# Optimization experiments

Measured on AMD Instinct MI355X. Metric: run time of the kernel, lower is better.

The kernel has to match this reference:

```python
import jax, jax.numpy as jnp
import numpy as np

B, T, C, H = 8, 1024, 1024, 16
D = C // H
EPS = 1e-5

def _ln(x, g, b):
    mu = jnp.mean(x, axis=-1, keepdims=True)
    var = jnp.var(x, axis=-1, keepdims=True)
    return (x - mu) * jax.lax.rsqrt(var + EPS) * g + b

def _build_mask(cond_mask, cond_len, token_len):
    # Vectorized form of the per-batch Python-loop mask in the torch module.
    counts = jnp.sum(cond_mask, axis=-1)            # [B] number of valid cond tokens
    rows = jnp.arange(T)
    cols = jnp.arange(T)
    # all rows may attend to the first counts[i] (cond) columns
    m_cond = cols[None, None, :] < counts[:, None, None]          # [B,1,T]
    m_cond = jnp.broadcast_to(m_cond, (B, T, T))
    # block-causal tiled pattern on rows/cols >= cond_len:
    # value = (col - cond_len) % token_len <= (row - cond_len) % token_len
    pattern = ((cols[None, :] - cond_len) % token_len) <= ((rows[:, None] - cond_len) % token_len)
    m_block = (rows[:, None] >= cond_len) & (cols[None, :] >= cond_len) & pattern  # [T,T]
    # cols >= cond_len: overwritten by block pattern (rows < cond_len stay 0 there)
    mask = jnp.where(cols[None, None, :] < cond_len, m_cond, m_block[None, :, :])
    return mask[:, None, :, :]                      # [B,1,T,T] bool

def _attn(x, Wq, bq, Wk, bk, Wv, bv, Wp, bp, cond_mask, cond_len, token_len):
    q = (x @ Wq + bq).reshape(B, T, H, D).transpose(0, 2, 1, 3)  # [B,H,T,D]
    k = (x @ Wk + bk).reshape(B, T, H, D).transpose(0, 2, 1, 3)
    v = (x @ Wv + bv).reshape(B, T, H, D).transpose(0, 2, 1, 3)
    att = jnp.einsum('bhqd,bhkd->bhqk', q, k) * (1.0 / np.sqrt(D))
    mask = _build_mask(cond_mask, cond_len, token_len)
    att = jnp.where(mask, att, -jnp.inf)
    att = jax.nn.softmax(att, axis=-1)
    y = jnp.einsum('bhqk,bhkd->bhqd', att, v)
    y = y.transpose(0, 2, 1, 3).reshape(B, T, C)
    return y @ Wp + bp

def setup_inputs() -> dict:
    key = jax.random.key(0)
    ks = jax.random.split(key, 16)
    cond_len, token_len = 256, 768
    s = 1.0 / np.sqrt(C)
    counts = jax.random.randint(ks[0], (B,), 1, cond_len + 1)
    cond_mask = (jnp.arange(T)[None, :] < counts[:, None]).astype(jnp.int32)
    return {
        'x': jax.random.normal(ks[1], (B, T, C), jnp.float32),
        'ln1_g': jnp.ones((C,), jnp.float32), 'ln1_b': jnp.zeros((C,), jnp.float32),
        'Wq': jax.random.normal(ks[2], (C, C), jnp.float32) * s, 'bq': jnp.zeros((C,), jnp.float32),
        'Wk': jax.random.normal(ks[3], (C, C), jnp.float32) * s, 'bk': jnp.zeros((C,), jnp.float32),
        'Wv': jax.random.normal(ks[4], (C, C), jnp.float32) * s, 'bv': jnp.zeros((C,), jnp.float32),
        'Wp': jax.random.normal(ks[5], (C, C), jnp.float32) * s, 'bp': jnp.zeros((C,), jnp.float32),
        'ln2_g': jnp.ones((C,), jnp.float32), 'ln2_b': jnp.zeros((C,), jnp.float32),
        'W1': jax.random.normal(ks[6], (C, 4 * C), jnp.float32) * s, 'b1': jnp.zeros((4 * C,), jnp.float32),
        'W2': jax.random.normal(ks[7], (4 * C, C), jnp.float32) * (0.5 * s), 'b2': jnp.zeros((C,), jnp.float32),
        'cond_mask': cond_mask,
        'cond_len': cond_len,
        'token_len': token_len,
    }

def reference(x, ln1_g, ln1_b, Wq, bq, Wk, bk, Wv, bv, Wp, bp, ln2_g, ln2_b, W1, b1, W2, b2, cond_mask, cond_len, token_len):
    x = x + _attn(_ln(x, ln1_g, ln1_b), Wq, bq, Wk, bk, Wv, bv, Wp, bp, cond_mask, cond_len, token_len)
    h = _ln(x, ln2_g, ln2_b)
    x = x + (jax.nn.gelu(h @ W1 + b1, approximate=False) @ W2 + b2)
    return x
```

## Files before the change

kernel.cpp:

```cpp
#include <hip/hip_runtime.h>
#include <hip/hip_bf16.h>
#include <cstdint>
#include <cstddef>

typedef __attribute__((ext_vector_type(8))) short short8;
typedef __attribute__((ext_vector_type(4))) float f32x4;
typedef __attribute__((ext_vector_type(4))) unsigned short us4;

#define MFMA_BF16(a, b, c) __builtin_amdgcn_mfma_f32_16x16x32_bf16((a), (b), (c), 0, 0, 0)
#define VMCNT(n) asm volatile("s_waitcnt vmcnt(" #n ")" ::: "memory")

__device__ __forceinline__ unsigned short f2bf(float f) {
  unsigned int u = __float_as_uint(f);
  u += 0x7FFFu + ((u >> 16) & 1u);
  return (unsigned short)(u >> 16);
}

__device__ __forceinline__ float gelu_fast(float v) {
  const float u = v * (0.79788456f + 0.03567741f * v * v);
  const float e = exp2f(u * 2.88539008f);
  return v - v * __builtin_amdgcn_rcpf(e + 1.0f);
}

typedef const void __attribute__((address_space(1)))* as1_cvp;
typedef void __attribute__((address_space(3)))* as3_vp;
__device__ __forceinline__ void gll16(const short* g, short* l) {
#if defined(__HIP_DEVICE_COMPILE__)
  __builtin_amdgcn_global_load_lds((as1_cvp)g, (as3_vp)l, 16, 0, 0);
#else
  (void)g; (void)l;
#endif
}

__global__ void count_kernel(const int* __restrict__ cm, int* __restrict__ counts) {
  __shared__ int sd[256];
  const int b = blockIdx.x, t = threadIdx.x;
  int s = 0;
  for (int i = t; i < 1024; i += 256) s += cm[b * 1024 + i];
  sd[t] = s; __syncthreads();
  for (int k = 128; k > 0; k >>= 1) { if (t < k) sd[t] += sd[t + k]; __syncthreads(); }
  if (t == 0) counts[b] = sd[0];
}

__global__ void pack_bias_kernel(const float* __restrict__ bq, const float* __restrict__ bk,
                                 const float* __restrict__ bv, float* __restrict__ dst) {
  int i = blockIdx.x * 256 + threadIdx.x;
  dst[i] = (i < 1024) ? bq[i] : (i < 2048 ? bk[i - 1024] : bv[i - 2048]);
}

__global__ void transpose_kernel(const float* __restrict__ src, unsigned short* __restrict__ dst,
                                 int R, int C) {
  __shared__ float tile[32][33];
  const int c0 = blockIdx.x * 32, r0 = blockIdx.y * 32;
  const int tx = threadIdx.x, ty = threadIdx.y;
  #pragma unroll
  for (int i = ty; i < 32; i += 8)
    tile[i][tx] = src[(size_t)(r0 + i) * C + (c0 + tx)];
  __syncthreads();
  #pragma unroll
  for (int i = ty; i < 32; i += 8)
    dst[(size_t)(c0 + i) * R + (r0 + tx)] = f2bf(tile[tx][i]);
}

__global__ void vtrans_kernel(const short* __restrict__ qkv, short* __restrict__ vtr) {
  __shared__ short tile[32][33];
  const int bh = blockIdx.z;
  const int t0 = blockIdx.x * 32, d0 = blockIdx.y * 32;
  const int b = bh >> 4, h = bh & 15;
  const int tx = threadIdx.x, ty = threadIdx.y;
  const short* src = qkv + (size_t)b * 1024 * 3072 + 2048 + h * 64;
  #pragma unroll
  for (int i = ty; i < 32; i += 8)
    tile[i][tx] = src[(size_t)(t0 + i) * 3072 + d0 + tx];
  __syncthreads();
  short* dst = vtr + (size_t)bh * 65536;
  #pragma unroll
  for (int i = ty; i < 32; i += 8)
    dst[(d0 + i) * 1024 + t0 + tx] = tile[tx][i];
}

__global__ __launch_bounds__(256) void ln_kernel(const float* __restrict__ in,
                                                 const float* __restrict__ gw,
                                                 const float* __restrict__ bw,
                                                 unsigned short* __restrict__ out) {
  const int row = blockIdx.x, t = threadIdx.x;
  const float4 v = ((const float4*)(in + (size_t)row * 1024))[t];
  float s = v.x + v.y + v.z + v.w;
  float ss = v.x * v.x + v.y * v.y + v.z * v.z + v.w * v.w;
  #pragma unroll
  for (int o = 32; o >= 1; o >>= 1) { s += __shfl_down(s, o, 64); ss += __shfl_down(ss, o, 64); }
  __shared__ float red[8];
  if ((t & 63) == 0) { red[t >> 6] = s; red[4 + (t >> 6)] = ss; }
  __syncthreads();
  const float S  = red[0] + red[1] + red[2] + red[3];
  const float SS = red[4] + red[5] + red[6] + red[7];
  const float mu = S * (1.0f / 1024.0f);
  const float var = SS * (1.0f / 1024.0f) - mu * mu;
  const float rs = rsqrtf(var + 1e-5f);
  const int c = t * 4;
  const float4 g4 = ((const float4*)gw)[t];
  const float4 b4 = ((const float4*)bw)[t];
  us4 o4;
  o4[0] = f2bf((v.x - mu) * rs * g4.x + b4.x);
  o4[1] = f2bf((v.y - mu) * rs * g4.y + b4.y);
  o4[2] = f2bf((v.z - mu) * rs * g4.z + b4.z);
  o4[3] = f2bf((v.w - mu) * rs * g4.w + b4.w);
  *(us4*)(out + (size_t)row * 1024 + c) = o4;
}

template <int EPI>
__global__ __launch_bounds__(512, 1) void gemm_n256_kernel(
    const short* __restrict__ A, const short* __restrict__ BT,
    const float* __restrict__ bias, int N, int K, int gm,
    unsigned short* __restrict__ outb) {
  __shared__ alignas(16) short lds[73728];
  const int t = threadIdx.x;
  const int l = t & 63, w = t >> 6;
  const int lq = l & 15, g = l >> 4;
  const int wr = w >> 2, wc = w & 3;
  const int cpx = (int)gridDim.x >> 3;
  const int wid = ((int)blockIdx.x & 7) * cpx + ((int)blockIdx.x >> 3);
  const int bm = (wid % gm) * 128, bn = (wid / gm) * 256;
  const int NT = K >> 6;

  const int csw = ((t & 7) ^ ((t >> 3) & 7)) * 8;
  const int sr = t >> 3;

  const f32x4 z4 = {0.f, 0.f, 0.f, 0.f};
  f32x4 acc[4][4];
  #pragma unroll
  for (int i = 0; i < 4; i++)
    #pragma unroll
    for (int j = 0; j < 4; j++) acc[i][j] = z4;

  auto stageA = [&](int buf, int k0) {
    const short* src = A + (size_t)(bm + sr) * K + k0 + csw;
    short* dst = lds + buf * 24576 + t * 8;
    gll16(src, dst);
    gll16(src + (size_t)64 * K, dst + 4096);
  };
  auto stageB = [&](int buf, int h, int k0) {
    const short* src = BT + (size_t)(bn + h * 128 + sr) * K + k0 + csw;
    short* dst = lds + buf * 24576 + 8192 + h * 8192 + t * 8;
    gll16(src, dst);
    gll16(src + (size_t)64 * K, dst + 4096);
  };
  auto rdA = [&](int buf, int mi2, int kk) {
    const int ra = wr * 64 + mi2 * 16 + lq;
    const int unit = (kk * 4 + g) ^ (ra & 7);
    return *(const short8*)(lds + buf * 24576 + ra * 64 + unit * 8);
  };
  auto rdB = [&](int buf, int h, int ni2, int kk) {
    const int cb = wc * 32 + ni2 * 16 + lq;
    const int unit = (kk * 4 + g) ^ (cb & 7);
    return *(const short8*)(lds + buf * 24576 + 8192 + h * 8192 + cb * 64 + unit * 8);
  };

  stageA(0, 0);     stageB(0, 0, 0);
  stageB(0, 1, 0);
  stageA(1, 64);    stageB(1, 0, 64);
  VMCNT(4);
  __builtin_amdgcn_s_barrier();

  int cur = 0;
  for (int v = 0; v < NT; ++v) {
    const int nx1 = (cur == 2) ? 0 : cur + 1;
    const int nx2 = (nx1 == 2) ? 0 : nx1 + 1;
    short8 a[4][2], b[2][2], b2[2][2];
    #pragma unroll
    for (int mi2 = 0; mi2 < 4; ++mi2)
      #pragma unroll
      for (int kk = 0; kk < 2; ++kk) a[mi2][kk] = rdA(cur, mi2, kk);
    #pragma unroll
    for (int ni2 = 0; ni2 < 2; ++ni2)
      #pragma unroll
      for (int kk = 0; kk < 2; ++kk) b[ni2][kk] = rdB(cur, 0, ni2, kk);
    if (v + 1 < NT) stageB(nx1, 1, (v + 1) * 64);
    __builtin_amdgcn_s_setprio(1);
    #pragma unroll
    for (int mi2 = 0; mi2 < 4; ++mi2)
      #pragma unroll
      for (int ni2 = 0; ni2 < 2; ++ni2)
        #pragma unroll
        for (int kk = 0; kk < 2; ++kk)
          acc[mi2][ni2] = MFMA_BF16(a[mi2][kk], b[ni2][kk], acc[mi2][ni2]);
    __builtin_amdgcn_s_setprio(0);
    #pragma unroll
    for (int ni2 = 0; ni2 < 2; ++ni2)
      #pragma unroll
      for (int kk = 0; kk < 2; ++kk) b2[ni2][kk] = rdB(cur, 1, ni2, kk);
    if (v + 2 < NT) {
      stageA(nx2, (v + 2) * 64); stageB(nx2, 0, (v + 2) * 64);
      VMCNT(4);
    } else {
      VMCNT(0);
    }
    __builtin_amdgcn_s_barrier();
    __builtin_amdgcn_s_setprio(1);
    #pragma unroll
    for (int mi2 = 0; mi2 < 4; ++mi2)
      #pragma unroll
      for (int ni2 = 0; ni2 < 2; ++ni2)
        #pragma unroll
        for (int kk = 0; kk < 2; ++kk)
          acc[mi2][2 + ni2] = MFMA_BF16(a[mi2][kk], b2[ni2][kk], acc[mi2][2 + ni2]);
    __builtin_amdgcn_s_setprio(0);
    cur = nx1;
  }

  __syncthreads();
  unsigned short* eb = (unsigned short*)lds;
  #pragma unroll
  for (int mi2 = 0; mi2 < 4; ++mi2) {
    #pragma unroll
    for (int n = 0; n < 4; ++n) {
      const int col = (n >> 1) * 128 + wc * 32 + (n & 1) * 16 + lq;
      const float bv = bias[bn + col];
      #pragma unroll
      for (int r = 0; r < 4; ++r) {
        const int row = wr * 64 + mi2 * 16 + 4 * g + r;
        float vv = acc[mi2][n][r] + bv;
        if (EPI == 1) vv = gelu_fast(vv);
        eb[row * 256 + col] = f2bf(vv);
      }
    }
  }
  __syncthreads();
  #pragma unroll
  for (int it = 0; it < 8; ++it) {
    const int unit = it * 512 + t;
    const int row = unit >> 5, c8 = unit & 31;
    const short8 vv = *(const short8*)(lds + unit * 8);
    *(short8*)((short*)outb + (size_t)(bm + row) * N + bn + c8 * 8) = vv;
  }
}

template <int EPI>
__global__ __launch_bounds__(512, 1) void gemm_k2_kernel(
    const short* __restrict__ A, const short* __restrict__ BT,
    const float* __restrict__ bias, int N, int K, int gm,
    float* __restrict__ outf, const float* __restrict__ res) {
  __shared__ alignas(16) short lds[73728];
  const int t = threadIdx.x;
  const int l = t & 63, w = t >> 6;
  const int lq = l & 15, g = l >> 4;
  const int wr = w >> 2, wc = w & 3;
  const int cpx = (int)gridDim.x >> 3;
  const int wid = ((int)blockIdx.x & 7) * cpx + ((int)blockIdx.x >> 3);
  const int bm = (wid % gm) * 256, bn = (wid / gm) * 128;
  const int NT = K >> 6;

  const int csw = ((t & 7) ^ ((t >> 3) & 7)) * 8;
  const int sA = t >> 3;
  const int sB = ((t >> 8) & 1) * 64 + ((t >> 3) & 31);

  const f32x4 z4 = {0.f, 0.f, 0.f, 0.f};
  f32x4 acc[8][2];
  #pragma unroll
  for (int i = 0; i < 8; i++) { acc[i][0] = z4; acc[i][1] = z4; }

  auto stageA = [&](int buf, int h, int k0) {
    const short* src = A + (size_t)(bm + h * 64 + sA) * K + k0 + csw;
    short* dst = lds + buf * 24576 + h * 8192 + t * 8;
    gll16(src, dst);
    gll16(src + (size_t)128 * K, dst + 4096);
  };
  auto stageB = [&](int buf, int h, int k0) {
    const short* src = BT + (size_t)(bn + h * 32 + sB) * K + k0 + csw;
    short* dst = lds + buf * 24576 + 16384 + h * 4096 + t * 8;
    gll16(src, dst);
  };
  auto rdA = [&](int buf, int mh, int mi2, int kk) {
    const int ra = wr * 64 + mi2 * 16 + lq;
    const int unit = (kk * 4 + g) ^ (ra & 7);
    return *(const short8*)(lds + buf * 24576 + mh * 8192 + ra * 64 + unit * 8);
  };
  auto rdB = [&](int buf, int ni2, int kk) {
    const int h = wc & 1;
    const int rb = (wc >> 1) * 32 + ni2 * 16 + lq;
    const int unit = (kk * 4 + g) ^ (rb & 7);
    return *(const short8*)(lds + buf * 24576 + 16384 + h * 4096 + rb * 64 + unit * 8);
  };

  stageA(0, 0, 0);  stageB(0, 0, 0);
  stageA(0, 1, 0);  stageB(0, 1, 0);
  stageA(1, 0, 64); stageB(1, 0, 64);
  VMCNT(3);
  __builtin_amdgcn_s_barrier();

  int cur = 0;
  for (int v = 0; v < NT; ++v) {
    const int nx1 = (cur == 2) ? 0 : cur + 1;
    const int nx2 = (nx1 == 2) ? 0 : nx1 + 1;
    short8 a[4][2], b[2][2], a2[4][2];
    #pragma unroll
    for (int mi2 = 0; mi2 < 4; ++mi2)
      #pragma unroll
      for (int kk = 0; kk < 2; ++kk) a[mi2][kk] = rdA(cur, 0, mi2, kk);
    #pragma unroll
    for (int ni2 = 0; ni2 < 2; ++ni2)
      #pragma unroll
      for (int kk = 0; kk < 2; ++kk) b[ni2][kk] = rdB(cur, ni2, kk);
    if (v + 1 < NT) { stageA(nx1, 1, (v + 1) * 64); stageB(nx1, 1, (v + 1) * 64); }
    __builtin_amdgcn_s_setprio(1);
    #pragma unroll
    for (int mi2 = 0; mi2 < 4; ++mi2)
      #pragma unroll
      for (int ni2 = 0; ni2 < 2; ++ni2)
        #pragma unroll
        for (int kk = 0; kk < 2; ++kk)
          acc[mi2][ni2] = MFMA_BF16(a[mi2][kk], b[ni2][kk], acc[mi2][ni2]);
    __builtin_amdgcn_s_setprio(0);
    #pragma unroll
    for (int mi2 = 0; mi2 < 4; ++mi2)
      #pragma unroll
      for (int kk = 0; kk < 2; ++kk) a2[mi2][kk] = rdA(cur, 1, mi2, kk);
    if (v + 2 < NT) {
      stageA(nx2, 0, (v + 2) * 64); stageB(nx2, 0, (v + 2) * 64);
      VMCNT(3);
    } else {
      VMCNT(0);
    }
    __builtin_amdgcn_s_barrier();
    __builtin_amdgcn_s_setprio(1);
    #pragma unroll
    for (int mi2 = 0; mi2 < 4; ++mi2)
      #pragma unroll
      for (int ni2 = 0; ni2 < 2; ++ni2)
        #pragma unroll
        for (int kk = 0; kk < 2; ++kk)
          acc[4 + mi2][ni2] = MFMA_BF16(a2[mi2][kk], b[ni2][kk], acc[4 + mi2][ni2]);
    __builtin_amdgcn_s_setprio(0);
    cur = nx1;
  }

  #pragma unroll
  for (int mi = 0; mi < 8; ++mi) {
    #pragma unroll
    for (int ni = 0; ni < 2; ++ni) {
      const int col = bn + wc * 32 + ni * 16 + lq;
      const float bv = bias[col];
      #pragma unroll
      for (int r = 0; r < 4; ++r) {
        const int row = bm + wr * 128 + (mi >> 2) * 64 + (mi & 3) * 16 + 4 * g + r;
        const size_t idx = (size_t)row * N + col;
        outf[idx] = acc[mi][ni][r] + bv + res[idx];
      }
    }
  }
}

__global__ __launch_bounds__(64) void attn_kernel(
    const short* __restrict__ qkv, const short* __restrict__ vtr,
    unsigned short* __restrict__ y, const int* __restrict__ counts) {
  const int blk = blockIdx.x;
  const int slot = blk >> 3;
  const int p = slot & 31;
  const int bh = ((slot >> 5) << 3) | (blk & 7);
  const int b = bh >> 4, h = bh & 15;
  const int l = threadIdx.x & 63;
  const int lq = l & 15, g = l >> 4;
  const int qb0 = p * 16, qb1 = (63 - p) * 16;
  const int count = counts[b];

  const short* base  = qkv + (size_t)b * 1024 * 3072 + h * 64;
  const short* vbase = vtr + (size_t)bh * 65536;

  short8 qf[2][2];
  {
    const short* qr0 = base + (size_t)(qb0 + lq) * 3072 + 8 * g;
    const short* qr1 = base + (size_t)(qb1 + lq) * 3072 + 8 * g;
    qf[0][0] = *(const short8*)qr0; qf[0][1] = *(const short8*)(qr0 + 32);
    qf[1][0] = *(const short8*)qr1; qf[1][1] = *(const short8*)(qr1 + 32);
  }

  const f32x4 z4 = {0.f, 0.f, 0.f, 0.f};
  f32x4 oacc[2][4];
  #pragma unroll
  for (int grp = 0; grp < 2; ++grp)
    #pragma unroll
    for (int dc = 0; dc < 4; ++dc) oacc[grp][dc] = z4;
  float mrun[2] = {-1e30f, -1e30f};
  float lrun[2] = {0.f, 0.f};
  const int permrow = 8 * (lq >> 2) + (lq & 3);
  const float SC = 0.125f * 1.44269504088896f;

  const int ncond = min((count + 31) >> 5, 8);
  const int ncausal = (qb1 + 16 - 256 + 31) >> 5;
  const int nt = ncond + ncausal;
  auto kv_of = [&](int i) { return i < ncond ? i * 32 : 256 + (i - ncond) * 32; };

  auto loadt = [&](int kv0, short8 (&kr)[4], short8 (&vr)[4]) {
    const short* ka = base + (size_t)(kv0 + permrow) * 3072 + 1024 + 8 * g;
    kr[0] = *(const short8*)ka;
    kr[1] = *(const short8*)(ka + 32);
    kr[2] = *(const short8*)(ka + 4 * 3072);
    kr[3] = *(const short8*)(ka + 4 * 3072 + 32);
    #pragma unroll
    for (int dc = 0; dc < 4; ++dc)
      vr[dc] = *(const short8*)(vbase + (16 * dc + lq) * 1024 + kv0 + 8 * g);
  };

  auto compute = [&](int i, const short8 (&kr)[4], const short8 (&vr)[4]) {
    const int kv0 = kv_of(i);
    const bool isCond = (i < ncond);
    #pragma unroll
    for (int grp = 0; grp < 2; ++grp) {
      const int qb = grp ? qb1 : qb0;
      if (!isCond && kv0 >= qb + 16) continue;
      const bool needMask = isCond ? (kv0 + 32 > count) : (kv0 + 31 > qb);
      f32x4 sA = z4, sB = z4;
      __builtin_amdgcn_s_setprio(1);
      sA = MFMA_BF16(kr[0], qf[grp][0], sA);
      sA = MFMA_BF16(kr[1], qf[grp][1], sA);
      sB = MFMA_BF16(kr[2], qf[grp][0], sB);
      sB = MFMA_BF16(kr[3], qf[grp][1], sB);
      __builtin_amdgcn_s_setprio(0);
      const int q = qb + lq;
      float mx = -1e30f;
      if (needMask) {
        #pragma unroll
        for (int r = 0; r < 4; ++r) {
          const int colA = kv0 + 8 * g + r, colB = colA + 4;
          const bool okA = isCond ? (colA < count) : (colA <= q);
          const bool okB = isCond ? (colB < count) : (colB <= q);
          const float vA = okA ? sA[r] * SC : -1e30f;
          const float vB = okB ? sB[r] * SC : -1e30f;
          sA[r] = vA; sB[r] = vB;
          mx = fmaxf(fmaxf(vA, vB), mx);
        }
      } else {
        #pragma unroll
        for (int r = 0; r < 4; ++r) {
          const float vA = sA[r] * SC, vB = sB[r] * SC;
          sA[r] = vA; sB[r] = vB;
          mx = fmaxf(fmaxf(vA, vB), mx);
        }
      }
      mx = fmaxf(mx, __shfl_xor(mx, 16, 64));
      mx = fmaxf(mx, __shfl_xor(mx, 32, 64));
      float m = mrun[grp];
      if (!__all(mx <= m + 8.0f)) {
        const float mn = fmaxf(m, mx);
        const float sf = exp2f(m - mn);
        lrun[grp] *= sf;
        #pragma unroll
        for (int dc = 0; dc < 4; ++dc)
          #pragma unroll
          for (int r = 0; r < 4; ++r) oacc[grp][dc][r] *= sf;
        mrun[grp] = mn; m = mn;
      }
      float ps = 0.f;
      #pragma unroll
      for (int r = 0; r < 4; ++r) {
        const float aa = exp2f(sA[r] - m);
        const float c2 = exp2f(sB[r] - m);
        sA[r] = aa; sB[r] = c2; ps += aa + c2;
      }
      ps += __shfl_xor(ps, 16, 64);
      ps += __shfl_xor(ps, 32, 64);
      lrun[grp] += ps;
      union { short8 s8; __hip_bfloat162 h2[4]; } pu;
      pu.h2[0] = __float22bfloat162_rn(float2{sA[0], sA[1]});
      pu.h2[1] = __float22bfloat162_rn(float2{sA[2], sA[3]});
      pu.h2[2] = __float22bfloat162_rn(float2{sB[0], sB[1]});
      pu.h2[3] = __float22bfloat162_rn(float2{sB[2], sB[3]});
      __builtin_amdgcn_s_setprio(1);
      #pragma unroll
      for (int dc = 0; dc < 4; ++dc)
        oacc[grp][dc] = MFMA_BF16(vr[dc], pu.s8, oacc[grp][dc]);
      __builtin_amdgcn_s_setprio(0);
    }
  };

  short8 kb0[4], vb0[4], kb1[4], vb1[4];
  loadt(kv_of(0), kb0, vb0);
  for (int i = 0; i < nt; i += 2) {
    if (i + 1 < nt) loadt(kv_of(i + 1), kb1, vb1);
    compute(i, kb0, vb0);
    if (i + 1 >= nt) break;
    if (i + 2 < nt) loadt(kv_of(i + 2), kb0, vb0);
    compute(i + 1, kb1, vb1);
  }

  #pragma unroll
  for (int grp = 0; grp < 2; ++grp) {
    const int qb = grp ? qb1 : qb0;
    const float inv = 1.0f / lrun[grp];
    unsigned short* yr = y + (size_t)(b * 1024 + qb + lq) * 1024 + h * 64;
    #pragma unroll
    for (int dc = 0; dc < 4; ++dc)
      #pragma unroll
      for (int r = 0; r < 4; ++r)
        yr[16 * dc + 4 * g + r] = f2bf(oacc[grp][dc][r] * inv);
  }
}

extern "C" void kernel_launch(void* const* d_in, const int* in_sizes, int n_in,
                              void* d_out, int out_size, void* d_ws, size_t ws_size,
                              hipStream_t stream) {
  (void)in_sizes; (void)n_in; (void)out_size; (void)ws_size;
  const float* x     = (const float*)d_in[0];
  const float* ln1_g = (const float*)d_in[1];
  const float* ln1_b = (const float*)d_in[2];
  const float* Wq    = (const float*)d_in[3];
  const float* bq    = (const float*)d_in[4];
  const float* Wk    = (const float*)d_in[5];
  const float* bk    = (const float*)d_in[6];
  const float* Wv    = (const float*)d_in[7];
  const float* bv    = (const float*)d_in[8];
  const float* Wp    = (const float*)d_in[9];
  const float* bp    = (const float*)d_in[10];
  const float* ln2_g = (const float*)d_in[11];
  const float* ln2_b = (const float*)d_in[12];
  const float* W1    = (const float*)d_in[13];
  const float* b1    = (const float*)d_in[14];
  const float* W2    = (const float*)d_in[15];
  const float* b2    = (const float*)d_in[16];
  const int* cond_mask = (const int*)d_in[17];

  char* ws = (char*)d_ws;
  const size_t MB = 1u << 20;
  short* xn    = (short*)(ws + 0);
  short* vtr   = (short*)(ws + 0);
  short* qkv   = (short*)(ws + 16 * MB);
  short* act   = (short*)(ws + 0);
  unsigned short* yb = (unsigned short*)(ws + 64 * MB);
  float* x1    = (float*)(ws + 80 * MB);
  short* hb    = (short*)(ws + 112 * MB);
  short* wqkvT = (short*)(ws + 128 * MB);
  short* wpT   = (short*)(ws + 134 * MB);
  short* w1T   = (short*)(ws + 136 * MB);
  short* w2T   = (short*)(ws + 144 * MB);
  float* bqkv  = (float*)(ws + 152 * MB);
  int* counts  = (int*)(ws + 152 * MB + 16384);

  const dim3 tb(32, 8);
  count_kernel<<<8, 256, 0, stream>>>(cond_mask, counts);
  pack_bias_kernel<<<12, 256, 0, stream>>>(bq, bk, bv, bqkv);
  transpose_kernel<<<dim3(32, 32), tb, 0, stream>>>(Wq, (unsigned short*)wqkvT, 1024, 1024);
  transpose_kernel<<<dim3(32, 32), tb, 0, stream>>>(Wk, (unsigned short*)(wqkvT + 1024 * 1024), 1024, 1024);
  transpose_kernel<<<dim3(32, 32), tb, 0, stream>>>(Wv, (unsigned short*)(wqkvT + 2 * 1024 * 1024), 1024, 1024);
  transpose_kernel<<<dim3(32, 32), tb, 0, stream>>>(Wp, (unsigned short*)wpT, 1024, 1024);
  transpose_kernel<<<dim3(128, 32), tb, 0, stream>>>(W1, (unsigned short*)w1T, 1024, 4096);
  transpose_kernel<<<dim3(32, 128), tb, 0, stream>>>(W2, (unsigned short*)w2T, 4096, 1024);
  ln_kernel<<<8192, 256, 0, stream>>>(x, ln1_g, ln1_b, (unsigned short*)xn);

  gemm_n256_kernel<0><<<768, 512, 0, stream>>>(xn, wqkvT, bqkv, 3072, 1024, 64,
                                               (unsigned short*)qkv);
  vtrans_kernel<<<dim3(32, 2, 128), tb, 0, stream>>>(qkv, vtr);
  attn_kernel<<<4096, 64, 0, stream>>>(qkv, vtr, yb, counts);
  gemm_k2_kernel<2><<<256, 512, 0, stream>>>((const short*)yb, wpT, bp, 1024, 1024, 32,
                                             x1, x);
  ln_kernel<<<8192, 256, 0, stream>>>(x1, ln2_g, ln2_b, (unsigned short*)hb);
  gemm_n256_kernel<1><<<1024, 512, 0, stream>>>(hb, w1T, b1, 4096, 1024, 64,
                                                (unsigned short*)act);
  gemm_k2_kernel<2><<<256, 512, 0, stream>>>(act, w2T, b2, 1024, 4096, 32,
                                             (float*)d_out, x1);
}
```

Measured before the change: 440.5 us.

## Split paired query tiles into one 16-row tile per attention block

The attention kernel used to give each 64-thread block two 16-row query tiles, a short and a long one paired to balance causal work. Each block now handles a single query tile and the grid doubles to 8192 blocks. This cuts per-block register use and raises parallelism and occupancy. In exchange the K/V tiles shared by the two query groups are loaded twice, and blocks differ more in how much work they do.

```diff
diff --git a/kernel.cpp b/kernel.cpp
--- a/kernel.cpp
+++ b/kernel.cpp
@@ -355,38 +355,32 @@
     unsigned short* __restrict__ y, const int* __restrict__ counts) {
   const int blk = blockIdx.x;
   const int slot = blk >> 3;
-  const int p = slot & 31;
-  const int bh = ((slot >> 5) << 3) | (blk & 7);
+  const int qt = slot & 63;
+  const int bh = ((slot >> 6) << 3) | (blk & 7);
   const int b = bh >> 4, h = bh & 15;
   const int l = threadIdx.x & 63;
   const int lq = l & 15, g = l >> 4;
-  const int qb0 = p * 16, qb1 = (63 - p) * 16;
+  const int qb = qt * 16;
   const int count = counts[b];
 
   const short* base  = qkv + (size_t)b * 1024 * 3072 + h * 64;
   const short* vbase = vtr + (size_t)bh * 65536;
 
-  short8 qf[2][2];
+  short8 qf0, qf1;
   {
-    const short* qr0 = base + (size_t)(qb0 + lq) * 3072 + 8 * g;
-    const short* qr1 = base + (size_t)(qb1 + lq) * 3072 + 8 * g;
-    qf[0][0] = *(const short8*)qr0; qf[0][1] = *(const short8*)(qr0 + 32);
-    qf[1][0] = *(const short8*)qr1; qf[1][1] = *(const short8*)(qr1 + 32);
+    const short* qr = base + (size_t)(qb + lq) * 3072 + 8 * g;
+    qf0 = *(const short8*)qr;
+    qf1 = *(const short8*)(qr + 32);
   }
 
   const f32x4 z4 = {0.f, 0.f, 0.f, 0.f};
-  f32x4 oacc[2][4];
-  #pragma unroll
-  for (int grp = 0; grp < 2; ++grp)
-    #pragma unroll
-    for (int dc = 0; dc < 4; ++dc) oacc[grp][dc] = z4;
-  float mrun[2] = {-1e30f, -1e30f};
-  float lrun[2] = {0.f, 0.f};
+  f32x4 oacc[4] = {z4, z4, z4, z4};
+  float mrun = -1e30f, lrun = 0.f;
   const int permrow = 8 * (lq >> 2) + (lq & 3);
   const float SC = 0.125f * 1.44269504088896f;
 
   const int ncond = min((count + 31) >> 5, 8);
-  const int ncausal = (qb1 + 16 - 256 + 31) >> 5;
+  const int ncausal = (qb + 16 > 256) ? ((qb + 16 - 256 + 31) >> 5) : 0;
   const int nt = ncond + ncausal;
   auto kv_of = [&](int i) { return i < ncond ? i * 32 : 256 + (i - ncond) * 32; };
 
@@ -404,73 +398,68 @@
   auto compute = [&](int i, const short8 (&kr)[4], const short8 (&vr)[4]) {
     const int kv0 = kv_of(i);
     const bool isCond = (i < ncond);
-    #pragma unroll
-    for (int grp = 0; grp < 2; ++grp) {
-      const int qb = grp ? qb1 : qb0;
-      if (!isCond && kv0 >= qb + 16) continue;
-      const bool needMask = isCond ? (kv0 + 32 > count) : (kv0 + 31 > qb);
-      f32x4 sA = z4, sB = z4;
-      __builtin_amdgcn_s_setprio(1);
-      sA = MFMA_BF16(kr[0], qf[grp][0], sA);
-      sA = MFMA_BF16(kr[1], qf[grp][1], sA);
-      sB = MFMA_BF16(kr[2], qf[grp][0], sB);
-      sB = MFMA_BF16(kr[3], qf[grp][1], sB);
-      __builtin_amdgcn_s_setprio(0);
-      const int q = qb + lq;
-      float mx = -1e30f;
-      if (needMask) {
+    const bool needMask = isCond ? (kv0 + 32 > count) : (kv0 + 31 > qb);
+    f32x4 sA = z4, sB = z4;
+    __builtin_amdgcn_s_setprio(1);
+    sA = MFMA_BF16(kr[0], qf0, sA);
+    sA = MFMA_BF16(kr[1], qf1, sA);
+    sB = MFMA_BF16(kr[2], qf0, sB);
+    sB = MFMA_BF16(kr[3], qf1, sB);
+    __builtin_amdgcn_s_setprio(0);
+    const int q = qb + lq;
+    float mx = -1e30f;
+    if (needMask) {
+      #pragma unroll
+      for (int r = 0; r < 4; ++r) {
+        const int colA = kv0 + 8 * g + r, colB = colA + 4;
+        const bool okA = isCond ? (colA < count) : (colA <= q);
+        const bool okB = isCond ? (colB < count) : (colB <= q);
+        const float vA = okA ? sA[r] * SC : -1e30f;
+        const float vB = okB ? sB[r] * SC : -1e30f;
+        sA[r] = vA; sB[r] = vB;
+        mx = fmaxf(fmaxf(vA, vB), mx);
+      }
+    } else {
+      #pragma unroll
+      for (int r = 0; r < 4; ++r) {
+        const float vA = sA[r] * SC, vB = sB[r] * SC;
+        sA[r] = vA; sB[r] = vB;
+        mx = fmaxf(fmaxf(vA, vB), mx);
+      }
+    }
+    mx = fmaxf(mx, __shfl_xor(mx, 16, 64));
+    mx = fmaxf(mx, __shfl_xor(mx, 32, 64));
+    float m = mrun;
+    if (!__all(mx <= m + 8.0f)) {
+      const float mn = fmaxf(m, mx);
+      const float sf = exp2f(m - mn);
+      lrun *= sf;
+      #pragma unroll
+      for (int dc = 0; dc < 4; ++dc)
         #pragma unroll
-        for (int r = 0; r < 4; ++r) {
-          const int colA = kv0 + 8 * g + r, colB = colA + 4;
-          const bool okA = isCond ? (colA < count) : (colA <= q);
-          const bool okB = isCond ? (colB < count) : (colB <= q);
-          const float vA = okA ? sA[r] * SC : -1e30f;
-          const float vB = okB ? sB[r] * SC : -1e30f;
-          sA[r] = vA; sB[r] = vB;
-          mx = fmaxf(fmaxf(vA, vB), mx);
-        }
-      } else {
-        #pragma unroll
-        for (int r = 0; r < 4; ++r) {
-          const float vA = sA[r] * SC, vB = sB[r] * SC;
-          sA[r] = vA; sB[r] = vB;
-          mx = fmaxf(fmaxf(vA, vB), mx);
-        }
-      }
-      mx = fmaxf(mx, __shfl_xor(mx, 16, 64));
-      mx = fmaxf(mx, __shfl_xor(mx, 32, 64));
-      float m = mrun[grp];
-      if (!__all(mx <= m + 8.0f)) {
-        const float mn = fmaxf(m, mx);
-        const float sf = exp2f(m - mn);
-        lrun[grp] *= sf;
-        #pragma unroll
-        for (int dc = 0; dc < 4; ++dc)
-          #pragma unroll
-          for (int r = 0; r < 4; ++r) oacc[grp][dc][r] *= sf;
-        mrun[grp] = mn; m = mn;
-      }
-      float ps = 0.f;
-      #pragma unroll
-      for (int r = 0; r < 4; ++r) {
-        const float aa = exp2f(sA[r] - m);
-        const float c2 = exp2f(sB[r] - m);
-        sA[r] = aa; sB[r] = c2; ps += aa + c2;
-      }
-      ps += __shfl_xor(ps, 16, 64);
-      ps += __shfl_xor(ps, 32, 64);
-      lrun[grp] += ps;
-      union { short8 s8; __hip_bfloat162 h2[4]; } pu;
-      pu.h2[0] = __float22bfloat162_rn(float2{sA[0], sA[1]});
-      pu.h2[1] = __float22bfloat162_rn(float2{sA[2], sA[3]});
-      pu.h2[2] = __float22bfloat162_rn(float2{sB[0], sB[1]});
-      pu.h2[3] = __float22bfloat162_rn(float2{sB[2], sB[3]});
-      __builtin_amdgcn_s_setprio(1);
-      #pragma unroll
-      for (int dc = 0; dc < 4; ++dc)
-        oacc[grp][dc] = MFMA_BF16(vr[dc], pu.s8, oacc[grp][dc]);
-      __builtin_amdgcn_s_setprio(0);
-    }
+        for (int r = 0; r < 4; ++r) oacc[dc][r] *= sf;
+      mrun = mn; m = mn;
+    }
+    float ps = 0.f;
+    #pragma unroll
+    for (int r = 0; r < 4; ++r) {
+      const float aa = exp2f(sA[r] - m);
+      const float c2 = exp2f(sB[r] - m);
+      sA[r] = aa; sB[r] = c2; ps += aa + c2;
+    }
+    ps += __shfl_xor(ps, 16, 64);
+    ps += __shfl_xor(ps, 32, 64);
+    lrun += ps;
+    union { short8 s8; __hip_bfloat162 h2[4]; } pu;
+    pu.h2[0] = __float22bfloat162_rn(float2{sA[0], sA[1]});
+    pu.h2[1] = __float22bfloat162_rn(float2{sA[2], sA[3]});
+    pu.h2[2] = __float22bfloat162_rn(float2{sB[0], sB[1]});
+    pu.h2[3] = __float22bfloat162_rn(float2{sB[2], sB[3]});
+    __builtin_amdgcn_s_setprio(1);
+    #pragma unroll
+    for (int dc = 0; dc < 4; ++dc)
+      oacc[dc] = MFMA_BF16(vr[dc], pu.s8, oacc[dc]);
+    __builtin_amdgcn_s_setprio(0);
   };
 
   short8 kb0[4], vb0[4], kb1[4], vb1[4];
@@ -483,17 +472,13 @@
     compute(i + 1, kb1, vb1);
   }
 
-  #pragma unroll
-  for (int grp = 0; grp < 2; ++grp) {
-    const int qb = grp ? qb1 : qb0;
-    const float inv = 1.0f / lrun[grp];
-    unsigned short* yr = y + (size_t)(b * 1024 + qb + lq) * 1024 + h * 64;
-    #pragma unroll
-    for (int dc = 0; dc < 4; ++dc)
-      #pragma unroll
-      for (int r = 0; r < 4; ++r)
-        yr[16 * dc + 4 * g + r] = f2bf(oacc[grp][dc][r] * inv);
-  }
+  const float inv = 1.0f / lrun;
+  unsigned short* yr = y + (size_t)(b * 1024 + qb + lq) * 1024 + h * 64;
+  #pragma unroll
+  for (int dc = 0; dc < 4; ++dc)
+    #pragma unroll
+    for (int r = 0; r < 4; ++r)
+      yr[16 * dc + 4 * g + r] = f2bf(oacc[dc][r] * inv);
 }
 
 extern "C" void kernel_launch(void* const* d_in, const int* in_sizes, int n_in,
@@ -549,7 +534,7 @@
   gemm_n256_kernel<0><<<768, 512, 0, stream>>>(xn, wqkvT, bqkv, 3072, 1024, 64,
                                                (unsigned short*)qkv);
   vtrans_kernel<<<dim3(32, 2, 128), tb, 0, stream>>>(qkv, vtr);
-  attn_kernel<<<4096, 64, 0, stream>>>(qkv, vtr, yb, counts);
+  attn_kernel<<<8192, 64, 0, stream>>>(qkv, vtr, yb, counts);
   gemm_k2_kernel<2><<<256, 512, 0, stream>>>((const short*)yb, wpT, bp, 1024, 1024, 32,
                                              x1, x);
   ln_kernel<<<8192, 256, 0, stream>>>(x1, ln2_g, ln2_b, (unsigned short*)hb);
```

After: 469.9 us. 1.07x slower.
